# Kernel tuning notes

Measured on AMD Instinct MI355X. Metric: run time of the kernel, lower is better.

The kernel has to match this reference:

```python
import jax, jax.numpy as jnp
import numpy as np

NPOINT, RADIUS, NSAMPLE = 512, 0.2, 32
MLP = [64, 64, 128]
IN_CH = 67
EPS = 1e-5


def farthest_point_sample(xyz, npoint):
    # xyz: [B, N, 3] -> idx [B, npoint]. Deterministic start at index 0.
    B, N, _ = xyz.shape

    def step(carry, _):
        dist, far = carry  # dist [B,N], far [B]
        centroid = jnp.take_along_axis(xyz, far[:, None, None], axis=1)  # [B,1,3]
        d = jnp.sum((xyz - centroid) ** 2, axis=-1)  # [B,N]
        dist = jnp.minimum(dist, d)
        return (dist, jnp.argmax(dist, axis=-1).astype(jnp.int32)), far

    init = (jnp.full((B, N), 1e10, dtype=xyz.dtype), jnp.zeros((B,), jnp.int32))
    _, idxs = jax.lax.scan(step, init, None, length=npoint)
    return idxs.T  # [B, npoint]


def query_ball_point(radius, nsample, xyz, new_xyz):
    # xyz [B,N,3], new_xyz [B,S,3] -> idx [B,S,nsample]
    B, N, _ = xyz.shape
    sqr = jnp.sum((new_xyz[:, :, None, :] - xyz[:, None, :, :]) ** 2, axis=-1)  # [B,S,N]
    gidx = jnp.where(sqr > radius * radius, N, jnp.arange(N, dtype=jnp.int32))
    gidx = jnp.sort(gidx, axis=-1)[:, :, :nsample]
    first = gidx[:, :, :1]
    return jnp.where(gidx == N, first, gidx).astype(jnp.int32)


def gather_points(pts, idx):
    # pts [B,N,C], idx [B,...] -> [B,...,C]
    return jax.vmap(lambda p, i: p[i])(pts, idx)


def sample_and_group(npoint, radius, nsample, xyz, points):
    fps_idx = farthest_point_sample(xyz, npoint)          # [B,S]
    new_xyz = gather_points(xyz, fps_idx)                 # [B,S,3]
    idx = query_ball_point(radius, nsample, xyz, new_xyz)  # [B,S,K]
    grouped_xyz = gather_points(xyz, idx)                 # [B,S,K,3]
    grouped_xyz_norm = grouped_xyz - new_xyz[:, :, None, :]
    grouped_pts = gather_points(points, idx)              # [B,S,K,D]
    new_points = jnp.concatenate([grouped_xyz_norm, grouped_pts], axis=-1)  # [B,S,K,3+D]
    return new_xyz, new_points


def mlp_bn_relu(x, w, b, gamma, beta):
    # x [B,C,K,S]; 1x1 conv + training-mode BatchNorm2d + ReLU
    y = jnp.einsum('oc,bcks->boks', w, x) + b[None, :, None, None]
    mean = jnp.mean(y, axis=(0, 2, 3), keepdims=True)
    var = jnp.var(y, axis=(0, 2, 3), keepdims=True)
    y = (y - mean) * jax.lax.rsqrt(var + EPS)
    y = y * gamma[None, :, None, None] + beta[None, :, None, None]
    return jax.nn.relu(y)


def setup_inputs() -> dict:
    key = jax.random.key(0)
    ks = jax.random.split(key, 8)
    B, N, D = 16, 2048, 64
    inp = {
        'xyz': jax.random.normal(ks[0], (B, 3, N), jnp.float32),
        'points': jax.random.normal(ks[1], (B, D, N), jnp.float32),
    }
    last = IN_CH
    for i, out in enumerate(MLP):
        kw = jax.random.fold_in(ks[2], i)
        inp[f'w{i}'] = jax.random.normal(kw, (out, last), jnp.float32) * 0.05
        inp[f'b{i}'] = jnp.zeros((out,), jnp.float32)
        inp[f'g{i}'] = jnp.ones((out,), jnp.float32)
        inp[f'bt{i}'] = jnp.zeros((out,), jnp.float32)
        last = out
    return inp


def reference(xyz, points, w0, b0, g0, bt0, w1, b1, g1, bt1, w2, b2, g2, bt2):
    # xyz [B,3,N], points [B,D,N]
    xyz_t = jnp.transpose(xyz, (0, 2, 1))      # [B,N,3]
    pts_t = jnp.transpose(points, (0, 2, 1))   # [B,N,D]
    new_xyz, new_points = sample_and_group(NPOINT, RADIUS, NSAMPLE, xyz_t, pts_t)
    # [B,S,K,C] -> [B,C,K,S]
    x = jnp.transpose(new_points, (0, 3, 2, 1))
    for (w, b, g, bt) in ((w0, b0, g0, bt0), (w1, b1, g1, bt1), (w2, b2, g2, bt2)):
        x = mlp_bn_relu(x, w, b, g, bt)
    feature = jnp.max(x, axis=2)               # [B,C',S]
    new_xyz_out = jnp.transpose(new_xyz, (0, 2, 1))  # [B,3,S]
    return new_xyz_out, feature
```

## Files before the change

### kernel.cpp

```cpp
#include <hip/hip_runtime.h>
#include <hip/hip_bf16.h>
#include <stdint.h>

#define NB 16
#define NPT 2048
#define NS 512
#define NK 32
#define PTOT (NB*NS*NK)
#define EPSV 1e-5f

typedef __attribute__((ext_vector_type(8))) short short8;
typedef __attribute__((ext_vector_type(4))) float floatx4;

#define WS_NEWXYZ 0
#define WS_ST     24576
#define WS_W1BF   27136
#define WS_W2BF   29184
#define WS_W0R    33280
#define WS_RAWMAX 36352
#define WS_PTS_TB 560640
#define WS_Y1     1609216
#define WS_Y2     9997824

__device__ __forceinline__ float bf2f(ushort u){ return __uint_as_float((uint32_t)u<<16); }
__device__ __forceinline__ ushort f2bf(float f){
  uint32_t u = __float_as_uint(f);
  return (ushort)((u + 0x7FFFu + ((u>>16)&1u)) >> 16);
}

template<int CTRL>
__device__ __forceinline__ double dppmax64f(double k){
  long long b = __double_as_longlong(k);
  int lo = (int)(uint32_t)b, hi = (int)(b>>32);
  int olo = __builtin_amdgcn_update_dpp(lo, lo, CTRL, 0xF, 0xF, false);
  int ohi = __builtin_amdgcn_update_dpp(hi, hi, CTRL, 0xF, 0xF, false);
  double o = __hiloint2double(ohi, olo);
  return fmax(o, k);
}
__device__ __forceinline__ unsigned long long u64max(unsigned long long a, unsigned long long b){ return a>b?a:b; }

__global__ __launch_bounds__(256) void prep_kernel(const float* __restrict__ xyz,
    float* __restrict__ nxyz, float* __restrict__ out0,
    const float* __restrict__ pts, ushort* __restrict__ pts_tb,
    const float* __restrict__ w0, const float* __restrict__ w1, const float* __restrict__ w2,
    ushort* __restrict__ w0r, ushort* __restrict__ w1b, ushort* __restrict__ w2b,
    float* __restrict__ st)
{
  __shared__ union {
    struct { float4 lc[NPT]; double warr[2][4]; int sel[NS]; } f;
    float tile[64][65];
  } sm;
  const int blk = blockIdx.x;
  const int tid = threadIdx.x;
  if (blk < 16){
    const int b = blk;
    const float* xb = xyz + (size_t)b*3*NPT;
    float px[8], py[8], pz[8], dist[8];
    uint32_t lo_[8];
    #pragma unroll
    for (int j=0;j<8;j++){
      int n = j*256 + tid;
      float x = xb[n], y = xb[NPT+n], z = xb[2*NPT+n];
      sm.f.lc[n] = make_float4(x,y,z,0.f);
      px[j]=x; py[j]=y; pz[j]=z; dist[j]=1e10f;
      lo_[j] = ~(uint32_t)n;
    }
    if (tid==0) sm.f.sel[0]=0;
    __syncthreads();
    float4 c0 = sm.f.lc[0];
    float cx = c0.x, cy = c0.y, cz = c0.z;
    const int lane = tid & 63, wid = tid >> 6;
    for (int t=1;t<NS;t++){
      double kk[8];
      #pragma unroll
      for (int j=0;j<8;j++){
        float dx = __fsub_rn(px[j], cx);
        float dy = __fsub_rn(py[j], cy);
        float dz = __fsub_rn(pz[j], cz);
        float d  = __fadd_rn(__fadd_rn(__fmul_rn(dx,dx),__fmul_rn(dy,dy)),__fmul_rn(dz,dz));
        float dd = fminf(dist[j], d);
        dist[j] = dd;
        kk[j] = __hiloint2double((int)__float_as_uint(dd), (int)lo_[j]);
      }
      double m0 = fmax(kk[0],kk[1]), m1 = fmax(kk[2],kk[3]);
      double m2 = fmax(kk[4],kk[5]), m3 = fmax(kk[6],kk[7]);
      double best = fmax(fmax(m0,m1), fmax(m2,m3));
      best = dppmax64f<0xB1>(best);
      best = dppmax64f<0x4E>(best);
      best = dppmax64f<0x124>(best);
      best = dppmax64f<0x128>(best);
      long long bb = __double_as_longlong(best);
      int bl = (int)(uint32_t)bb, bh = (int)(bb>>32);
      unsigned long long k0 = (((unsigned long long)(uint32_t)__builtin_amdgcn_readlane(bh, 0))<<32)  | (uint32_t)__builtin_amdgcn_readlane(bl, 0);
      unsigned long long k1 = (((unsigned long long)(uint32_t)__builtin_amdgcn_readlane(bh, 16))<<32) | (uint32_t)__builtin_amdgcn_readlane(bl, 16);
      unsigned long long k2 = (((unsigned long long)(uint32_t)__builtin_amdgcn_readlane(bh, 32))<<32) | (uint32_t)__builtin_amdgcn_readlane(bl, 32);
      unsigned long long k3 = (((unsigned long long)(uint32_t)__builtin_amdgcn_readlane(bh, 48))<<32) | (uint32_t)__builtin_amdgcn_readlane(bl, 48);
      unsigned long long kw = u64max(u64max(k0,k1), u64max(k2,k3));
      if (lane==0) sm.f.warr[t&1][wid] = __longlong_as_double((long long)kw);
      __syncthreads();
      double w0_ = sm.f.warr[t&1][0], w1_ = sm.f.warr[t&1][1], w2_ = sm.f.warr[t&1][2], w3_ = sm.f.warr[t&1][3];
      double f = fmax(fmax(w0_,w1_), fmax(w2_,w3_));
      int n = (int)(~(uint32_t)__double_as_longlong(f));
      float4 cc = sm.f.lc[n];
      cx = cc.x; cy = cc.y; cz = cc.z;
      if (tid==0) sm.f.sel[t]=n;
    }
    __syncthreads();
    for (int s = tid; s < NS; s += 256){
      int n = sm.f.sel[s];
      float4 cc = sm.f.lc[n];
      float* np_ = nxyz + ((size_t)b*NS + s)*3;
      np_[0]=cc.x; np_[1]=cc.y; np_[2]=cc.z;
      float* ob = out0 + (size_t)b*3*NS + s;
      ob[0]=cc.x; ob[NS]=cc.y; ob[2*NS]=cc.z;
    }
  } else if (blk < 528){
    const int t2 = blk - 16;
    const int b = t2 >> 5;
    const int n0 = (t2 & 31) * 64;
    const int lane = tid & 63;
    const int row4 = tid >> 6;
    const float* src = pts + (size_t)b*64*NPT;
    #pragma unroll
    for (int r=0; r<16; r++){
      int cc = r*4 + row4;
      sm.tile[cc][lane] = src[(size_t)cc*NPT + n0 + lane];
    }
    __syncthreads();
    ushort* dst = pts_tb + ((size_t)b*NPT + n0)*64;
    #pragma unroll
    for (int r=0; r<16; r++){
      int nn = r*4 + row4;
      dst[(size_t)nn*64 + lane] = f2bf(sm.tile[lane][nn]);
    }
  } else {
    for (int i = tid; i < 4096; i += 256) w1b[i] = f2bf(w1[i]);
    for (int i = tid; i < 8192; i += 256) w2b[i] = f2bf(w2[i]);
    for (int i = tid; i < 2560; i += 256) st[i] = 0.f;
    for (int i = tid; i < 6144; i += 256){
      int o = i / 96, k = i - o*96;
      float v = (k < 64) ? w0[o*67 + 3 + k] : ((k < 67) ? w0[o*67 + (k-64)] : 0.f);
      w0r[i] = f2bf(v);
    }
  }
}

__global__ __launch_bounds__(256) void conv1_mfma(const float* __restrict__ xyz,
    const ushort* __restrict__ pts_tb, const float* __restrict__ nxyz,
    const ushort* __restrict__ w0r, const float* __restrict__ b0,
    ushort* __restrict__ y1)
{
  __shared__ int gq[4][NK];
  const int tid = threadIdx.x;
  const int wid = tid>>6, lane = tid&63;
  const int q = lane>>4, nn = lane&15;
  const int g = blockIdx.x*4 + wid;
  const int b = g >> 9;
  const float* xb = xyz + (size_t)b*3*NPT;
  const float* cgp = nxyz + (size_t)g*3;
  const float cx = cgp[0], cy = cgp[1], cz = cgp[2];
  {
    const float r2 = 0.2f*0.2f;
    int cnt = 0, first = 0;
    for (int ch=0; ch<NPT/64 && cnt<NK; ch++){
      int n = ch*64 + lane;
      float dx = __fsub_rn(cx, xb[n]);
      float dy = __fsub_rn(cy, xb[NPT+n]);
      float dz = __fsub_rn(cz, xb[2*NPT+n]);
      float d  = __fadd_rn(__fadd_rn(__fmul_rn(dx,dx),__fmul_rn(dy,dy)),__fmul_rn(dz,dz));
      bool in = (d <= r2);
      unsigned long long mask = __ballot(in);
      if (mask){
        if (cnt==0) first = ch*64 + (__ffsll((unsigned long long)mask)-1);
        if (in){
          int pos = cnt + __popcll(mask & ((1ull<<lane)-1ull));
          if (pos < NK) gq[wid][pos] = n;
        }
        cnt += __popcll(mask);
      }
    }
    if (cnt < NK && lane >= cnt && lane < NK) gq[wid][lane] = first;
  }
  int n0 = gq[wid][nn], n1 = gq[wid][16+nn];
  float dx0 = xb[n0]-cx, dy0 = xb[NPT+n0]-cy, dz0 = xb[2*NPT+n0]-cz;
  float dx1 = xb[n1]-cx, dy1 = xb[NPT+n1]-cy, dz1 = xb[2*NPT+n1]-cz;
  floatx4 z4 = {0.f,0.f,0.f,0.f};
  floatx4 acc[4][2];
  #pragma unroll
  for (int mt=0;mt<4;mt++){ acc[mt][0]=z4; acc[mt][1]=z4; }
  const ushort* pr0 = pts_tb + ((size_t)b*NPT + n0)*64;
  const ushort* pr1 = pts_tb + ((size_t)b*NPT + n1)*64;
  #pragma unroll
  for (int kh=0; kh<2; kh++){
    short8 B0 = *(const short8*)(pr0 + kh*32 + q*8);
    short8 B1 = *(const short8*)(pr1 + kh*32 + q*8);
    #pragma unroll
    for (int mt=0; mt<4; mt++){
      short8 A = *(const short8*)(w0r + (mt*16+nn)*96 + kh*32 + q*8);
      acc[mt][0] = __builtin_amdgcn_mfma_f32_16x16x32_bf16(A, B0, acc[mt][0], 0,0,0);
      acc[mt][1] = __builtin_amdgcn_mfma_f32_16x16x32_bf16(A, B1, acc[mt][1], 0,0,0);
    }
  }
  {
    short8 B0 = {0,0,0,0,0,0,0,0}, B1 = {0,0,0,0,0,0,0,0};
    if (q==0){
      B0[0]=(short)f2bf(dx0); B0[1]=(short)f2bf(dy0); B0[2]=(short)f2bf(dz0);
      B1[0]=(short)f2bf(dx1); B1[1]=(short)f2bf(dy1); B1[2]=(short)f2bf(dz1);
    }
    #pragma unroll
    for (int mt=0; mt<4; mt++){
      short8 A = *(const short8*)(w0r + (mt*16+nn)*96 + 64 + q*8);
      acc[mt][0] = __builtin_amdgcn_mfma_f32_16x16x32_bf16(A, B0, acc[mt][0], 0,0,0);
      acc[mt][1] = __builtin_amdgcn_mfma_f32_16x16x32_bf16(A, B1, acc[mt][1], 0,0,0);
    }
  }
  float bias_[4][4];
  #pragma unroll
  for (int mt=0;mt<4;mt++)
    #pragma unroll
    for (int r=0;r<4;r++) bias_[mt][r] = b0[mt*16 + q*4 + r];
  #pragma unroll
  for (int nt=0; nt<2; nt++){
    int p = g*32 + nt*16 + nn;
    #pragma unroll
    for (int mt=0; mt<4; mt++){
      float v0 = acc[mt][nt][0] + bias_[mt][0];
      float v1 = acc[mt][nt][1] + bias_[mt][1];
      float v2 = acc[mt][nt][2] + bias_[mt][2];
      float v3 = acc[mt][nt][3] + bias_[mt][3];
      uint2 wv;
      wv.x = (uint32_t)f2bf(v0) | ((uint32_t)f2bf(v1)<<16);
      wv.y = (uint32_t)f2bf(v2) | ((uint32_t)f2bf(v3)<<16);
      *(uint2*)(y1 + (size_t)p*64 + mt*16 + q*4) = wv;
    }
  }
}

__global__ __launch_bounds__(256) void stats64_kernel(const ushort* __restrict__ y,
                                                      float* __restrict__ stbase)
{
  const int wid = threadIdx.x>>6, lane = threadIdx.x&63;
  const int oct = lane & 7, pr = lane >> 3;
  const int p0 = blockIdx.x*1024 + wid*256;
  float s[8], s2[8];
  #pragma unroll
  for (int j=0;j<8;j++){ s[j]=0.f; s2[j]=0.f; }
  for (int it=0; it<32; it++){
    int p = p0 + it*8 + pr;
    short8 v = *(const short8*)(y + (size_t)p*64 + oct*8);
    #pragma unroll
    for (int j=0;j<8;j++){
      float f = bf2f((ushort)v[j]);
      s[j] += f; s2[j] = fmaf(f,f,s2[j]);
    }
  }
  #pragma unroll
  for (int off=8; off<64; off<<=1){
    #pragma unroll
    for (int j=0;j<8;j++){ s[j] += __shfl_xor(s[j],off,64); s2[j] += __shfl_xor(s2[j],off,64); }
  }
  __shared__ float sd[4][128];
  if (pr==0){
    #pragma unroll
    for (int j=0;j<8;j++){ sd[wid][oct*8+j] = s[j]; sd[wid][64+oct*8+j] = s2[j]; }
  }
  __syncthreads();
  int t = threadIdx.x;
  if (t < 128){
    float v = sd[0][t]+sd[1][t]+sd[2][t]+sd[3][t];
    int rep = blockIdx.x & 1;
    float* dst = (t<64) ? (stbase + rep*64 + t) : (stbase + 128 + rep*64 + (t-64));
    atomicAdd(dst, v);
  }
}

__global__ __launch_bounds__(256) void conv2_mfma(const ushort* __restrict__ yin,
    const float* __restrict__ st, const float* __restrict__ g0, const float* __restrict__ bt0,
    const ushort* __restrict__ Wb, const float* __restrict__ bias,
    ushort* __restrict__ yout)
{
  __shared__ float aAl[64], aBl[64];
  const int tid = threadIdx.x;
  if (tid < 64){
    float s = st[tid] + st[64+tid];
    float qv = st[128+tid] + st[192+tid];
    float mean = s * (1.f/PTOT);
    float var  = qv * (1.f/PTOT) - mean*mean;
    float a = g0[tid] * rsqrtf(var + EPSV);
    aAl[tid] = a;
    aBl[tid] = fmaf(-mean, a, bt0[tid]);
  }
  __syncthreads();
  const int wid = tid>>6, lane = tid&63;
  const int q = lane>>4, nn = lane&15;
  const int p0 = (blockIdx.x*4 + wid) * 32;
  float a_[2][8], b_[2][8];
  #pragma unroll
  for (int kh=0;kh<2;kh++)
    #pragma unroll
    for (int j=0;j<8;j++){
      a_[kh][j] = aAl[kh*32 + q*8 + j];
      b_[kh][j] = aBl[kh*32 + q*8 + j];
    }
  short8 Af[4][2];
  #pragma unroll
  for (int mt=0;mt<4;mt++)
    #pragma unroll
    for (int kh=0;kh<2;kh++)
      Af[mt][kh] = *(const short8*)(Wb + (mt*16 + nn)*64 + kh*32 + q*8);
  float bias_[4][4];
  #pragma unroll
  for (int mt=0;mt<4;mt++)
    #pragma unroll
    for (int r=0;r<4;r++) bias_[mt][r] = bias[mt*16 + q*4 + r];
  floatx4 z = {0.f,0.f,0.f,0.f};
  floatx4 acc[4][2];
  #pragma unroll
  for (int mt=0;mt<4;mt++){ acc[mt][0]=z; acc[mt][1]=z; }
  #pragma unroll
  for (int nt=0;nt<2;nt++){
    #pragma unroll
    for (int kh=0;kh<2;kh++){
      short8 raw = *(const short8*)(yin + (size_t)(p0 + nt*16 + nn)*64 + kh*32 + q*8);
      short8 bf;
      #pragma unroll
      for (int j=0;j<8;j++){
        float f = bf2f((ushort)raw[j]);
        f = fmaxf(fmaf(f, a_[kh][j], b_[kh][j]), 0.f);
        bf[j] = (short)f2bf(f);
      }
      #pragma unroll
      for (int mt=0;mt<4;mt++)
        acc[mt][nt] = __builtin_amdgcn_mfma_f32_16x16x32_bf16(Af[mt][kh], bf, acc[mt][nt], 0,0,0);
    }
  }
  #pragma unroll
  for (int nt=0;nt<2;nt++){
    int p = p0 + nt*16 + nn;
    #pragma unroll
    for (int mt=0;mt<4;mt++){
      float v0 = acc[mt][nt][0] + bias_[mt][0];
      float v1 = acc[mt][nt][1] + bias_[mt][1];
      float v2 = acc[mt][nt][2] + bias_[mt][2];
      float v3 = acc[mt][nt][3] + bias_[mt][3];
      uint2 w;
      w.x = (uint32_t)f2bf(v0) | ((uint32_t)f2bf(v1)<<16);
      w.y = (uint32_t)f2bf(v2) | ((uint32_t)f2bf(v3)<<16);
      *(uint2*)(yout + (size_t)p*64 + mt*16 + q*4) = w;
    }
  }
}

__global__ __launch_bounds__(256) void conv3_mfma(const ushort* __restrict__ yin,
    float* __restrict__ st, const float* __restrict__ g1, const float* __restrict__ bt1,
    const ushort* __restrict__ Wb, const float* __restrict__ bias,
    ushort* __restrict__ rawmax)
{
  __shared__ ushort tile[64*132];
  __shared__ float aAl[64], aBl[64];
  const int tid = threadIdx.x;
  if (tid < 64){
    float s = st[256+tid] + st[320+tid];
    float qv = st[384+tid] + st[448+tid];
    float mean = s * (1.f/PTOT);
    float var  = qv * (1.f/PTOT) - mean*mean;
    float a = g1[tid] * rsqrtf(var + EPSV);
    aAl[tid] = a;
    aBl[tid] = fmaf(-mean, a, bt1[tid]);
  }
  __syncthreads();
  const int wid = tid>>6, lane = tid&63;
  const int q = lane>>4, nn = lane&15;
  const int p0 = (blockIdx.x*4 + wid) * 16;
  float a_[2][8], b_[2][8];
  #pragma unroll
  for (int kh=0;kh<2;kh++)
    #pragma unroll
    for (int j=0;j<8;j++){
      a_[kh][j] = aAl[kh*32 + q*8 + j];
      b_[kh][j] = aBl[kh*32 + q*8 + j];
    }
  short8 bfr[2];
  #pragma unroll
  for (int kh=0;kh<2;kh++){
    short8 raw = *(const short8*)(yin + (size_t)(p0 + nn)*64 + kh*32 + q*8);
    short8 bf;
    #pragma unroll
    for (int j=0;j<8;j++){
      float f = bf2f((ushort)raw[j]);
      f = fmaxf(fmaf(f, a_[kh][j], b_[kh][j]), 0.f);
      bf[j] = (short)f2bf(f);
    }
    bfr[kh] = bf;
  }
  #pragma unroll 1
  for (int mh=0;mh<2;mh++){
    floatx4 z = {0.f,0.f,0.f,0.f};
    floatx4 acc[4];
    short8 Af[4][2];
    #pragma unroll
    for (int mt=0;mt<4;mt++){
      acc[mt]=z;
      #pragma unroll
      for (int kh=0;kh<2;kh++)
        Af[mt][kh] = *(const short8*)(Wb + ((mh*4+mt)*16 + nn)*64 + kh*32 + q*8);
    }
    #pragma unroll
    for (int kh=0;kh<2;kh++)
      #pragma unroll
      for (int mt=0;mt<4;mt++)
        acc[mt] = __builtin_amdgcn_mfma_f32_16x16x32_bf16(Af[mt][kh], bfr[kh], acc[mt], 0,0,0);
    #pragma unroll
    for (int mt=0;mt<4;mt++){
      int m0 = (mh*4+mt)*16;
      float v0 = acc[mt][0] + bias[m0 + q*4 + 0];
      float v1 = acc[mt][1] + bias[m0 + q*4 + 1];
      float v2 = acc[mt][2] + bias[m0 + q*4 + 2];
      float v3 = acc[mt][3] + bias[m0 + q*4 + 3];
      uint2 w;
      w.x = (uint32_t)f2bf(v0) | ((uint32_t)f2bf(v1)<<16);
      w.y = (uint32_t)f2bf(v2) | ((uint32_t)f2bf(v3)<<16);
      *(uint2*)&tile[(wid*16 + nn)*132 + m0 + q*4] = w;
    }
  }
  __syncthreads();
  const int c = tid >> 1, half = tid & 1;
  float s = 0.f, q2 = 0.f, mx = -1e30f;
  #pragma unroll 4
  for (int it=0; it<32; it++){
    float f = bf2f(tile[(half*32 + it)*132 + c]);
    s += f; q2 = fmaf(f,f,q2); mx = fmaxf(mx, f);
  }
  rawmax[(size_t)(blockIdx.x*2 + half)*128 + c] = f2bf(mx);
  s  += __shfl_xor(s, 1, 64);
  q2 += __shfl_xor(q2, 1, 64);
  if (half==0){
    int rep = blockIdx.x & 7;
    atomicAdd(&st[512  + rep*128 + c], s);
    atomicAdd(&st[1536 + rep*128 + c], q2);
  }
}

__global__ __launch_bounds__(256) void finalize_kernel(const ushort* __restrict__ rawmax,
    const float* __restrict__ st, const float* __restrict__ g2, const float* __restrict__ bt2,
    float* __restrict__ out)
{
  __shared__ float tile[64][65];
  __shared__ float aAl[128], aBl[128];
  const int tid = threadIdx.x;
  if (tid < 128){
    float s=0.f, qv=0.f;
    #pragma unroll
    for (int r=0;r<8;r++){ s += st[512 + r*128 + tid]; qv += st[1536 + r*128 + tid]; }
    float mean = s * (1.f/PTOT);
    float var  = qv * (1.f/PTOT) - mean*mean;
    float a = g2[tid] * rsqrtf(var + EPSV);
    aAl[tid] = a;
    aBl[tid] = fmaf(-mean, a, bt2[tid]);
  }
  __syncthreads();
  const int b  = blockIdx.x >> 4;
  const int ct = (blockIdx.x >> 3) & 1;
  const int stt = blockIdx.x & 7;
  const int c0 = ct*64, s0 = stt*64;
  const int lane = tid & 63, wid = tid >> 6;
  #pragma unroll
  for (int r=0;r<16;r++){
    int sl = r*4 + wid;
    tile[sl][lane] = bf2f(rawmax[((size_t)(b*512 + s0 + sl))*128 + c0 + lane]);
  }
  __syncthreads();
  #pragma unroll
  for (int r=0;r<16;r++){
    int cl = r*4 + wid;
    float a = aAl[c0+cl], bb = aBl[c0+cl];
    out[((size_t)(b*128 + c0 + cl))*512 + s0 + lane] = fmaxf(fmaf(tile[lane][cl], a, bb), 0.f);
  }
}

extern "C" void kernel_launch(void* const* d_in, const int* in_sizes, int n_in,
                              void* d_out, int out_size, void* d_ws, size_t ws_size,
                              hipStream_t stream) {
  const float* xyz = (const float*)d_in[0];
  const float* pts = (const float*)d_in[1];
  const float* w0  = (const float*)d_in[2];
  const float* b0  = (const float*)d_in[3];
  const float* g0  = (const float*)d_in[4];
  const float* bt0 = (const float*)d_in[5];
  const float* w1  = (const float*)d_in[6];
  const float* b1  = (const float*)d_in[7];
  const float* g1  = (const float*)d_in[8];
  const float* bt1 = (const float*)d_in[9];
  const float* w2  = (const float*)d_in[10];
  const float* b2  = (const float*)d_in[11];
  const float* g2  = (const float*)d_in[12];
  const float* bt2 = (const float*)d_in[13];
  float* out = (float*)d_out;
  float* ws  = (float*)d_ws;

  float* nxyz = ws + WS_NEWXYZ;
  float* st   = ws + WS_ST;
  ushort* w0r = (ushort*)(ws + WS_W0R);
  ushort* w1b = (ushort*)(ws + WS_W1BF);
  ushort* w2b = (ushort*)(ws + WS_W2BF);
  ushort* rawmax = (ushort*)(ws + WS_RAWMAX);
  ushort* pts_tb = (ushort*)(ws + WS_PTS_TB);
  ushort* y1 = (ushort*)(ws + WS_Y1);
  ushort* y2 = (ushort*)(ws + WS_Y2);

  prep_kernel<<<529,256,0,stream>>>(xyz, nxyz, out, pts, pts_tb, w0, w1, w2, w0r, w1b, w2b, st);
  conv1_mfma<<<2048,256,0,stream>>>(xyz, pts_tb, nxyz, w0r, b0, y1);
  stats64_kernel<<<256,256,0,stream>>>(y1, st);
  conv2_mfma<<<2048,256,0,stream>>>(y1, st, g0, bt0, w1b, b1, y2);
  stats64_kernel<<<256,256,0,stream>>>(y2, st + 256);
  conv3_mfma<<<4096,256,0,stream>>>(y2, st, g1, bt1, w2b, b2, rawmax);
  finalize_kernel<<<256,256,0,stream>>>(rawmax, st, g2, bt2, out + NB*3*NS);
}
```

Baseline: 430.2 us.

## Fuse BatchNorm statistics into conv1 and conv2 epilogues, drop stats kernels

Accumulates per-channel sum and sum-of-squares in the conv1 and conv2 epilogues from the fp32 pre-rounding values, reduces them with DPP row sums and shared memory, and atomically adds into 16 replicated slots. This removes two stats64 launches that each re-read the full bf16 activation buffers. The stats buffer and workspace offsets grow to hold the replicas. Stats now come from unrounded values, which slightly changes numerics, and each block issues more atomics.

```diff
diff --git a/kernel.cpp b/kernel.cpp
--- a/kernel.cpp
+++ b/kernel.cpp
@@ -14,13 +14,13 @@
 
 #define WS_NEWXYZ 0
 #define WS_ST     24576
-#define WS_W1BF   27136
-#define WS_W2BF   29184
-#define WS_W0R    33280
-#define WS_RAWMAX 36352
-#define WS_PTS_TB 560640
-#define WS_Y1     1609216
-#define WS_Y2     9997824
+#define WS_W1BF   30720
+#define WS_W2BF   32768
+#define WS_W0R    36864
+#define WS_RAWMAX 39936
+#define WS_PTS_TB 564224
+#define WS_Y1     1612800
+#define WS_Y2     10001408
 
 __device__ __forceinline__ float bf2f(ushort u){ return __uint_as_float((uint32_t)u<<16); }
 __device__ __forceinline__ ushort f2bf(float f){
@@ -38,6 +38,19 @@
   return fmax(o, k);
 }
 __device__ __forceinline__ unsigned long long u64max(unsigned long long a, unsigned long long b){ return a>b?a:b; }
+
+template<int CTRL>
+__device__ __forceinline__ float dppaddf(float v){
+  int o = __builtin_amdgcn_update_dpp(__float_as_int(v), __float_as_int(v), CTRL, 0xF, 0xF, false);
+  return v + __int_as_float(o);
+}
+__device__ __forceinline__ float rowsum16(float v){
+  v = dppaddf<0xB1>(v);
+  v = dppaddf<0x4E>(v);
+  v = dppaddf<0x124>(v);
+  v = dppaddf<0x128>(v);
+  return v;
+}
 
 __global__ __launch_bounds__(256) void prep_kernel(const float* __restrict__ xyz,
     float* __restrict__ nxyz, float* __restrict__ out0,
@@ -136,7 +149,7 @@
   } else {
     for (int i = tid; i < 4096; i += 256) w1b[i] = f2bf(w1[i]);
     for (int i = tid; i < 8192; i += 256) w2b[i] = f2bf(w2[i]);
-    for (int i = tid; i < 2560; i += 256) st[i] = 0.f;
+    for (int i = tid; i < 6144; i += 256) st[i] = 0.f;
     for (int i = tid; i < 6144; i += 256){
       int o = i / 96, k = i - o*96;
       float v = (k < 64) ? w0[o*67 + 3 + k] : ((k < 67) ? w0[o*67 + (k-64)] : 0.f);
@@ -148,9 +161,10 @@
 __global__ __launch_bounds__(256) void conv1_mfma(const float* __restrict__ xyz,
     const ushort* __restrict__ pts_tb, const float* __restrict__ nxyz,
     const ushort* __restrict__ w0r, const float* __restrict__ b0,
-    ushort* __restrict__ y1)
+    ushort* __restrict__ y1, float* __restrict__ st)
 {
   __shared__ int gq[4][NK];
+  __shared__ float lsum[4][64], lsq[4][64];
   const int tid = threadIdx.x;
   const int wid = tid>>6, lane = tid&63;
   const int q = lane>>4, nn = lane&15;
@@ -214,76 +228,59 @@
       acc[mt][1] = __builtin_amdgcn_mfma_f32_16x16x32_bf16(A, B1, acc[mt][1], 0,0,0);
     }
   }
-  float bias_[4][4];
+  float ss[4][4], sq2[4][4];
   #pragma unroll
   for (int mt=0;mt<4;mt++)
     #pragma unroll
-    for (int r=0;r<4;r++) bias_[mt][r] = b0[mt*16 + q*4 + r];
+    for (int r=0;r<4;r++){ ss[mt][r]=0.f; sq2[mt][r]=0.f; }
   #pragma unroll
   for (int nt=0; nt<2; nt++){
     int p = g*32 + nt*16 + nn;
     #pragma unroll
     for (int mt=0; mt<4; mt++){
-      float v0 = acc[mt][nt][0] + bias_[mt][0];
-      float v1 = acc[mt][nt][1] + bias_[mt][1];
-      float v2 = acc[mt][nt][2] + bias_[mt][2];
-      float v3 = acc[mt][nt][3] + bias_[mt][3];
+      float v0 = acc[mt][nt][0] + b0[mt*16 + q*4 + 0];
+      float v1 = acc[mt][nt][1] + b0[mt*16 + q*4 + 1];
+      float v2 = acc[mt][nt][2] + b0[mt*16 + q*4 + 2];
+      float v3 = acc[mt][nt][3] + b0[mt*16 + q*4 + 3];
+      ss[mt][0]+=v0; ss[mt][1]+=v1; ss[mt][2]+=v2; ss[mt][3]+=v3;
+      sq2[mt][0]=fmaf(v0,v0,sq2[mt][0]); sq2[mt][1]=fmaf(v1,v1,sq2[mt][1]);
+      sq2[mt][2]=fmaf(v2,v2,sq2[mt][2]); sq2[mt][3]=fmaf(v3,v3,sq2[mt][3]);
       uint2 wv;
       wv.x = (uint32_t)f2bf(v0) | ((uint32_t)f2bf(v1)<<16);
       wv.y = (uint32_t)f2bf(v2) | ((uint32_t)f2bf(v3)<<16);
       *(uint2*)(y1 + (size_t)p*64 + mt*16 + q*4) = wv;
     }
   }
-}
-
-__global__ __launch_bounds__(256) void stats64_kernel(const ushort* __restrict__ y,
-                                                      float* __restrict__ stbase)
-{
-  const int wid = threadIdx.x>>6, lane = threadIdx.x&63;
-  const int oct = lane & 7, pr = lane >> 3;
-  const int p0 = blockIdx.x*1024 + wid*256;
-  float s[8], s2[8];
-  #pragma unroll
-  for (int j=0;j<8;j++){ s[j]=0.f; s2[j]=0.f; }
-  for (int it=0; it<32; it++){
-    int p = p0 + it*8 + pr;
-    short8 v = *(const short8*)(y + (size_t)p*64 + oct*8);
-    #pragma unroll
-    for (int j=0;j<8;j++){
-      float f = bf2f((ushort)v[j]);
-      s[j] += f; s2[j] = fmaf(f,f,s2[j]);
-    }
-  }
-  #pragma unroll
-  for (int off=8; off<64; off<<=1){
-    #pragma unroll
-    for (int j=0;j<8;j++){ s[j] += __shfl_xor(s[j],off,64); s2[j] += __shfl_xor(s2[j],off,64); }
-  }
-  __shared__ float sd[4][128];
-  if (pr==0){
-    #pragma unroll
-    for (int j=0;j<8;j++){ sd[wid][oct*8+j] = s[j]; sd[wid][64+oct*8+j] = s2[j]; }
-  }
-  __syncthreads();
-  int t = threadIdx.x;
-  if (t < 128){
-    float v = sd[0][t]+sd[1][t]+sd[2][t]+sd[3][t];
-    int rep = blockIdx.x & 1;
-    float* dst = (t<64) ? (stbase + rep*64 + t) : (stbase + 128 + rep*64 + (t-64));
-    atomicAdd(dst, v);
+  #pragma unroll
+  for (int mt=0;mt<4;mt++)
+    #pragma unroll
+    for (int r=0;r<4;r++){
+      float sv = rowsum16(ss[mt][r]);
+      float qv = rowsum16(sq2[mt][r]);
+      if (nn==0){ lsum[wid][mt*16+q*4+r] = sv; lsq[wid][mt*16+q*4+r] = qv; }
+    }
+  __syncthreads();
+  if (tid < 64){
+    float s = lsum[0][tid]+lsum[1][tid]+lsum[2][tid]+lsum[3][tid];
+    float q2v = lsq[0][tid]+lsq[1][tid]+lsq[2][tid]+lsq[3][tid];
+    int rep = blockIdx.x & 15;
+    atomicAdd(&st[rep*128 + tid], s);
+    atomicAdd(&st[rep*128 + 64 + tid], q2v);
   }
 }
 
 __global__ __launch_bounds__(256) void conv2_mfma(const ushort* __restrict__ yin,
-    const float* __restrict__ st, const float* __restrict__ g0, const float* __restrict__ bt0,
+    float* __restrict__ st, const float* __restrict__ g0, const float* __restrict__ bt0,
     const ushort* __restrict__ Wb, const float* __restrict__ bias,
     ushort* __restrict__ yout)
 {
   __shared__ float aAl[64], aBl[64];
+  __shared__ float lsum[4][64], lsq[4][64];
   const int tid = threadIdx.x;
   if (tid < 64){
-    float s = st[tid] + st[64+tid];
-    float qv = st[128+tid] + st[192+tid];
+    float s=0.f, qv=0.f;
+    #pragma unroll
+    for (int r=0;r<16;r++){ s += st[r*128 + tid]; qv += st[r*128 + 64 + tid]; }
     float mean = s * (1.f/PTOT);
     float var  = qv * (1.f/PTOT) - mean*mean;
     float a = g0[tid] * rsqrtf(var + EPSV);
@@ -334,6 +331,11 @@
         acc[mt][nt] = __builtin_amdgcn_mfma_f32_16x16x32_bf16(Af[mt][kh], bf, acc[mt][nt], 0,0,0);
     }
   }
+  float ss[4][4], sq2[4][4];
+  #pragma unroll
+  for (int mt=0;mt<4;mt++)
+    #pragma unroll
+    for (int r=0;r<4;r++){ ss[mt][r]=0.f; sq2[mt][r]=0.f; }
   #pragma unroll
   for (int nt=0;nt<2;nt++){
     int p = p0 + nt*16 + nn;
@@ -343,11 +345,30 @@
       float v1 = acc[mt][nt][1] + bias_[mt][1];
       float v2 = acc[mt][nt][2] + bias_[mt][2];
       float v3 = acc[mt][nt][3] + bias_[mt][3];
+      ss[mt][0]+=v0; ss[mt][1]+=v1; ss[mt][2]+=v2; ss[mt][3]+=v3;
+      sq2[mt][0]=fmaf(v0,v0,sq2[mt][0]); sq2[mt][1]=fmaf(v1,v1,sq2[mt][1]);
+      sq2[mt][2]=fmaf(v2,v2,sq2[mt][2]); sq2[mt][3]=fmaf(v3,v3,sq2[mt][3]);
       uint2 w;
       w.x = (uint32_t)f2bf(v0) | ((uint32_t)f2bf(v1)<<16);
       w.y = (uint32_t)f2bf(v2) | ((uint32_t)f2bf(v3)<<16);
       *(uint2*)(yout + (size_t)p*64 + mt*16 + q*4) = w;
     }
+  }
+  #pragma unroll
+  for (int mt=0;mt<4;mt++)
+    #pragma unroll
+    for (int r=0;r<4;r++){
+      float sv = rowsum16(ss[mt][r]);
+      float qv = rowsum16(sq2[mt][r]);
+      if (nn==0){ lsum[wid][mt*16+q*4+r] = sv; lsq[wid][mt*16+q*4+r] = qv; }
+    }
+  __syncthreads();
+  if (tid < 64){
+    float s = lsum[0][tid]+lsum[1][tid]+lsum[2][tid]+lsum[3][tid];
+    float q2v = lsq[0][tid]+lsq[1][tid]+lsq[2][tid]+lsq[3][tid];
+    int rep = blockIdx.x & 15;
+    atomicAdd(&st[2048 + rep*128 + tid], s);
+    atomicAdd(&st[2048 + rep*128 + 64 + tid], q2v);
   }
 }
 
@@ -360,8 +381,9 @@
   __shared__ float aAl[64], aBl[64];
   const int tid = threadIdx.x;
   if (tid < 64){
-    float s = st[256+tid] + st[320+tid];
-    float qv = st[384+tid] + st[448+tid];
+    float s=0.f, qv=0.f;
+    #pragma unroll
+    for (int r=0;r<16;r++){ s += st[2048 + r*128 + tid]; qv += st[2048 + r*128 + 64 + tid]; }
     float mean = s * (1.f/PTOT);
     float var  = qv * (1.f/PTOT) - mean*mean;
     float a = g1[tid] * rsqrtf(var + EPSV);
@@ -436,8 +458,8 @@
   q2 += __shfl_xor(q2, 1, 64);
   if (half==0){
     int rep = blockIdx.x & 7;
-    atomicAdd(&st[512  + rep*128 + c], s);
-    atomicAdd(&st[1536 + rep*128 + c], q2);
+    atomicAdd(&st[4096 + rep*128 + c], s);
+    atomicAdd(&st[5120 + rep*128 + c], q2);
   }
 }
 
@@ -451,7 +473,7 @@
   if (tid < 128){
     float s=0.f, qv=0.f;
     #pragma unroll
-    for (int r=0;r<8;r++){ s += st[512 + r*128 + tid]; qv += st[1536 + r*128 + tid]; }
+    for (int r=0;r<8;r++){ s += st[4096 + r*128 + tid]; qv += st[5120 + r*128 + tid]; }
     float mean = s * (1.f/PTOT);
     float var  = qv * (1.f/PTOT) - mean*mean;
     float a = g2[tid] * rsqrtf(var + EPSV);
@@ -509,10 +531,8 @@
   ushort* y2 = (ushort*)(ws + WS_Y2);
 
   prep_kernel<<<529,256,0,stream>>>(xyz, nxyz, out, pts, pts_tb, w0, w1, w2, w0r, w1b, w2b, st);
-  conv1_mfma<<<2048,256,0,stream>>>(xyz, pts_tb, nxyz, w0r, b0, y1);
-  stats64_kernel<<<256,256,0,stream>>>(y1, st);
+  conv1_mfma<<<2048,256,0,stream>>>(xyz, pts_tb, nxyz, w0r, b0, y1, st);
   conv2_mfma<<<2048,256,0,stream>>>(y1, st, g0, bt0, w1b, b1, y2);
-  stats64_kernel<<<256,256,0,stream>>>(y2, st + 256);
   conv3_mfma<<<4096,256,0,stream>>>(y2, st, g1, bt1, w2b, b2, rawmax);
   finalize_kernel<<<256,256,0,stream>>>(rawmax, st, g2, bt2, out + NB*3*NS);
 }
```

Result: no change. 427.4 us (-0.7%).
